# Kernel tuning notes

Measured on AMD Instinct MI355X. Metric: run time of the kernel, lower is better.

The kernel has to match this reference:

```python
import jax, jax.numpy as jnp
import numpy as np
import math

B, L, D = 2, 2048, 768
H, DK = 8, 64
DV = D // H  # 96
N_POS = 32
DFF = 2 * D
EPS = 1e-5


def setup_inputs() -> dict:
    key = jax.random.key(0)
    ks = jax.random.split(key, 12)
    s = 0.02
    return {
        "x": jax.random.normal(ks[0], (B, L, D), jnp.float32),
        "norm1_w": jnp.ones((D,), jnp.float32),
        "norm2_w": jnp.ones((D,), jnp.float32),
        "wq": jax.random.normal(ks[1], (D, H * DK), jnp.float32) * s,
        "wk": jax.random.normal(ks[2], (D, H * DK), jnp.float32) * s,
        "wv": jax.random.normal(ks[3], (D, H * DV), jnp.float32) * s,
        "wo": jax.random.normal(ks[4], (H * DV, D), jnp.float32) * s,
        "bo": jnp.zeros((D,), jnp.float32),
        "u_param": jax.random.normal(ks[5], (H, DK), jnp.float32) * s,
        "v_param": jax.random.normal(ks[6], (H, DK), jnp.float32) * s,
        "w_pos": jax.random.normal(ks[7], (H, DK, N_POS), jnp.float32) * s,
        "w1": jax.random.normal(ks[8], (D, DFF), jnp.float32) * s,
        "b1": jnp.zeros((DFF,), jnp.float32),
        "w2": jax.random.normal(ks[9], (DFF, D), jnp.float32) * s,
        "b2": jnp.zeros((D,), jnp.float32),
    }


def _rel_basis(l: int, n: int) -> jnp.ndarray:
    # Enformer-style central-mask relative position basis: [l, l, n]
    pos = jnp.arange(l)
    distance = pos[None, :] - pos[:, None]  # [l, l]
    pow_rate = jnp.exp(jnp.log(jnp.float32((l + 1) / 2.0)) / (n // 2))
    center_widths = pow_rate ** jnp.arange(1, n // 2 + 1, dtype=jnp.float32)
    d = distance[:, :, None].astype(jnp.float32)
    unsigned = (jnp.abs(d) <= center_widths).astype(jnp.float32)
    signed = jnp.sign(d) * unsigned
    return jnp.concatenate([unsigned, signed], axis=-1)  # [l, l, n]


def _rmsnorm(x, w):
    norm = jnp.mean(x * x, axis=-1, keepdims=True)
    return x * jax.lax.rsqrt(norm + EPS) * w


def reference(x, norm1_w, norm2_w, wq, wk, wv, wo, bo,
              u_param, v_param, w_pos, w1, b1, w2, b2):
    b, l, _ = x.shape
    skip = x
    h1 = _rmsnorm(x, norm1_w)

    q = (h1 @ wq).reshape(b, l, H, DK)
    k = (h1 @ wk).reshape(b, l, H, DK)
    v = (h1 @ wv).reshape(b, l, H, DV)

    basis = _rel_basis(l, N_POS)  # [l, l, n]
    scale = 1.0 / math.sqrt(DK)

    # qr_term: contract q with w_pos first, then with basis (avoids [h,l,l,d] r)
    qw = jnp.einsum('bihd,hdn->bihn', q, w_pos)          # [b,l,h,n]
    qr = jnp.einsum('bihn,ijn->bhij', qw, basis)          # [b,h,l,l]
    uk = jnp.einsum('hd,bjhd->bhj', u_param, k)[:, :, None, :]  # [b,h,1,l]
    vw = jnp.einsum('hd,hdn->hn', v_param, w_pos)         # [h,n]
    vr = jnp.einsum('hn,ijn->hij', vw, basis)[None]       # [1,h,l,l]

    bias = (qr + uk + vr) * scale
    scores = jnp.einsum('bihd,bjhd->bhij', q, k) * scale + bias
    attn = jax.nn.softmax(scores, axis=-1)
    out = jnp.einsum('bhij,bjhd->bihd', attn, v)          # [b,l,h,dv]

    out = out.reshape(b, l, H * DV) @ wo + bo
    x = out + skip

    skip = x
    h2 = _rmsnorm(x, norm2_w)
    h2 = jax.nn.gelu(h2 @ w1 + b1, approximate=False) @ w2 + b2
    return h2 + skip
```

## Files before the change

kernel.cpp:

```cpp
#include <hip/hip_runtime.h>

#define B_ 2
#define L_ 2048
#define D_ 768
#define H_ 8
#define DK_ 64
#define DV_ 96
#define NPOS_ 32

typedef __attribute__((ext_vector_type(8))) __bf16 bf16x8;
typedef __attribute__((ext_vector_type(4))) __bf16 bf16x4;
typedef __attribute__((ext_vector_type(4))) float f32x4;

static __device__ __forceinline__ float bs2f(short s) {
    return (float)__builtin_bit_cast(__bf16, s);
}
static __device__ __forceinline__ short f2bs(float f) {
    return __builtin_bit_cast(short, (__bf16)f);
}

typedef __attribute__((address_space(1))) void gas_void;
typedef __attribute__((address_space(3))) void las_void;
static __device__ __forceinline__ void gload16(const short* g, char* l) {
    __builtin_amdgcn_global_load_lds((const gas_void*)g, (las_void*)l, 16, 0, 0);
}

__global__ __launch_bounds__(256) void prep_kernel(
    const float* __restrict__ wq, const float* __restrict__ wk,
    const float* __restrict__ wv, const float* __restrict__ wo,
    const float* __restrict__ w1, const float* __restrict__ w2,
    const float* __restrict__ vparam, const float* __restrict__ uparam,
    const float* __restrict__ wpos,
    short* __restrict__ wqkvT, short* __restrict__ woT,
    short* __restrict__ w1T, short* __restrict__ w2T,
    unsigned char* __restrict__ sidx, float* __restrict__ VU, float* __restrict__ VS,
    const float* __restrict__ x, const float* __restrict__ n1w, short* __restrict__ h1)
{
    __shared__ short T[64][66];
    __shared__ float vw[H_ * NPOS_];
    __shared__ float uw[H_ * NPOS_];
    __shared__ float red[4];
    int blk = blockIdx.x, tid = threadIdx.x;
    if (blk < 1056) {
        const float* W; short* Wt; int K, N, bx, by;
        if (blk < 96)       { W = wq; Wt = wqkvT;              K = 768;  N = 512;  int b = blk;       bx = b % 8;  by = b / 8; }
        else if (blk < 192) { W = wk; Wt = wqkvT + 512 * 768;  K = 768;  N = 512;  int b = blk - 96;  bx = b % 8;  by = b / 8; }
        else if (blk < 336) { W = wv; Wt = wqkvT + 1024 * 768; K = 768;  N = 768;  int b = blk - 192; bx = b % 12; by = b / 12; }
        else if (blk < 480) { W = wo; Wt = woT;                K = 768;  N = 768;  int b = blk - 336; bx = b % 12; by = b / 12; }
        else if (blk < 768) { W = w1; Wt = w1T;                K = 768;  N = 1536; int b = blk - 480; bx = b % 24; by = b / 24; }
        else                { W = w2; Wt = w2T;                K = 1536; N = 768;  int b = blk - 768; bx = b % 12; by = b / 12; }
        int n0 = bx << 6, k0 = by << 6;
        for (int idx = tid; idx < 4096; idx += 256) {
            int r = idx >> 6, c = idx & 63;
            T[c][r] = f2bs(W[(size_t)(k0 + r) * N + n0 + c]);
        }
        __syncthreads();
        for (int idx = tid; idx < 4096; idx += 256) {
            int r = idx >> 6, c = idx & 63;
            Wt[(size_t)(n0 + r) * K + k0 + c] = T[r][c];
        }
    } else if (blk == 1056) {
        float pr = expf(logf((L_ + 1) / 2.0f) / (NPOS_ / 2));
        if (tid < 16) vw[tid] = powf(pr, (float)(tid + 1));
        __syncthreads();
        for (int idx = tid; idx < 4095; idx += 256) {
            int d = idx - 2047;
            int ad = d < 0 ? -d : d;
            int c = 0;
#pragma unroll
            for (int m = 0; m < 16; ++m)
                if (vw[m] < (float)ad) c++;
            sidx[idx] = (unsigned char)(d > 0 ? c : (d < 0 ? 17 + c : 34));
        }
        __syncthreads();
        {
            int h = tid >> 5, n = tid & 31;
            float av = 0.f, au = 0.f;
            for (int d = 0; d < DK_; ++d) {
                float wp = wpos[(h * DK_ + d) * NPOS_ + n];
                av += vparam[h * DK_ + d] * wp;
                au += uparam[h * DK_ + d] * wp;
            }
            vw[tid] = av;
            uw[tid] = au;
        }
        __syncthreads();
        if (tid < H_ * 17) {
            int h = tid / 17, m = tid % 17;
            float su = 0.f, ss = 0.f;
            for (int t2 = m; t2 < 16; ++t2) {
                su += vw[h * NPOS_ + t2] - uw[h * NPOS_ + t2];
                ss += vw[h * NPOS_ + 16 + t2] - uw[h * NPOS_ + 16 + t2];
            }
            VU[h * 17 + m] = su * 0.125f;
            VS[h * 17 + m] = ss * 0.125f;
        }
    } else {
        int row = blk - 1057;
        const float* xr = x + (size_t)row * D_;
        float ss = 0.f;
        for (int c = tid; c < D_; c += 256) { float f = xr[c]; ss += f * f; }
        for (int msk = 1; msk < 64; msk <<= 1) ss += __shfl_xor(ss, msk);
        if ((tid & 63) == 0) red[tid >> 6] = ss;
        __syncthreads();
        float tot = red[0] + red[1] + red[2] + red[3];
        float sc = rsqrtf(tot * (1.f / D_) + 1e-5f);
        for (int c = tid; c < D_; c += 256)
            h1[(size_t)row * D_ + c] = f2bs(xr[c] * sc * n1w[c]);
    }
}

__global__ __launch_bounds__(256) void rmsnorm_kernel(
    const float* __restrict__ x, const float* __restrict__ wgt, short* __restrict__ out)
{
    int row = blockIdx.x, tid = threadIdx.x;
    __shared__ float red[4];
    const float* xr = x + (size_t)row * D_;
    float ss = 0.f;
    for (int c = tid; c < D_; c += 256) { float f = xr[c]; ss += f * f; }
    for (int msk = 1; msk < 64; msk <<= 1) ss += __shfl_xor(ss, msk);
    if ((tid & 63) == 0) red[tid >> 6] = ss;
    __syncthreads();
    float tot = red[0] + red[1] + red[2] + red[3];
    float sc = rsqrtf(tot * (1.f / D_) + 1e-5f);
    for (int c = tid; c < D_; c += 256)
        out[(size_t)row * D_ + c] = f2bs(xr[c] * sc * wgt[c]);
}

template<int BN>
__global__ __launch_bounds__(512, 4) void gemmx(
    const short* __restrict__ A, const short* __restrict__ Bt,
    const float* __restrict__ bias, const float* __restrict__ uadd,
    const float* __restrict__ resid, void* __restrict__ outp,
    int M, int N, int K, int act, int out_f32)
{
    constexpr int STRIDE = 16384 + BN * 128;
    __shared__ __align__(16) char ldsb[2 * STRIDE];
    int tid = threadIdx.x;
    int w = tid >> 6, lane = tid & 63, quad = lane >> 4, t = lane & 15;
    int wm = (w >> 1) << 5;
    int wn = (w & 1) * (BN / 2);
    int m0b = blockIdx.y << 7, n0b = blockIdx.x * BN;

    int srow = tid >> 3;
    int scol = ((tid & 7) ^ (srow & 7)) << 3;
    const short* aSrc0 = A + (size_t)(m0b + srow) * K + scol;
    const short* aSrc1 = A + (size_t)(m0b + 64 + srow) * K + scol;
    const short* bSrc0 = Bt + (size_t)(n0b + srow) * K + scol;
    const short* bSrc1 = Bt + (size_t)(n0b + 64 + srow) * K + scol;
    int wo1024 = w << 10;

    f32x4 acc[2][BN / 32] = {};

    gload16(aSrc0, ldsb + wo1024);
    gload16(aSrc1, ldsb + 8192 + wo1024);
    gload16(bSrc0, ldsb + 16384 + wo1024);
    if (BN == 128) gload16(bSrc1, ldsb + 16384 + 8192 + wo1024);

    int swz = (t & 7) << 4;
    int cur = 0;
    for (int kb = 0; kb < K; kb += 64) {
        __syncthreads();
        if (kb + 64 < K) {
            char* nb = ldsb + (cur ^ 1) * STRIDE;
            gload16(aSrc0 + kb + 64, nb + wo1024);
            gload16(aSrc1 + kb + 64, nb + 8192 + wo1024);
            gload16(bSrc0 + kb + 64, nb + 16384 + wo1024);
            if (BN == 128) gload16(bSrc1 + kb + 64, nb + 16384 + 8192 + wo1024);
        }
        char* Ab = ldsb + cur * STRIDE;
        char* Bb = Ab + 16384;
#pragma unroll
        for (int ks = 0; ks < 2; ++ks) {
            int cb = ((ks << 6) + (quad << 4)) ^ swz;
            bf16x8 af[2], bf[BN / 32];
#pragma unroll
            for (int ms = 0; ms < 2; ++ms)
                af[ms] = *(const bf16x8*)(Ab + (wm + ms * 16 + t) * 128 + cb);
#pragma unroll
            for (int ns = 0; ns < BN / 32; ++ns)
                bf[ns] = *(const bf16x8*)(Bb + (wn + ns * 16 + t) * 128 + cb);
#pragma unroll
            for (int ms = 0; ms < 2; ++ms)
#pragma unroll
                for (int ns = 0; ns < BN / 32; ++ns)
                    acc[ms][ns] = __builtin_amdgcn_mfma_f32_16x16x32_bf16(af[ms], bf[ns], acc[ms][ns], 0, 0, 0);
        }
        cur ^= 1;
    }
#pragma unroll
    for (int ms = 0; ms < 2; ++ms)
#pragma unroll
        for (int ns = 0; ns < BN / 32; ++ns)
#pragma unroll
            for (int r = 0; r < 4; ++r) {
                int row = m0b + wm + ms * 16 + (quad << 2) + r;
                int col = n0b + wn + ns * 16 + t;
                float v2 = acc[ms][ns][r];
                if (uadd && col < 512) v2 = 0.125f * (v2 + uadd[col]);
                if (bias) v2 += bias[col];
                if (act == 1) v2 = 0.5f * v2 * (1.f + erff(v2 * 0.70710678118654752f));
                if (resid) v2 += resid[(size_t)row * N + col];
                if (out_f32) ((float*)outp)[(size_t)row * N + col] = v2;
                else ((short*)outp)[(size_t)row * N + col] = f2bs(v2);
            }
}

__global__ __launch_bounds__(256) void qv_kernel(
    const short* __restrict__ qkv, const float* __restrict__ wpos,
    const float* __restrict__ VU, const float* __restrict__ VS,
    float* __restrict__ Tg, short* __restrict__ vT, short* __restrict__ kT)
{
    __shared__ __align__(16) char arena[69696];
    int blk = blockIdx.x, tid = threadIdx.x;
    if (blk < 512) {
        float* qw = (float*)arena;
        float* sU = (float*)(arena + 1024);
        float* sS = (float*)(arena + 1568);
        int h = tid >> 5, n = tid & 31;
        float wlr[64];
#pragma unroll
        for (int d = 0; d < DK_; ++d)
            wlr[d] = wpos[(h * DK_ + d) * NPOS_ + n];
        int r0 = blk << 3;
        for (int rr = 0; rr < 8; ++rr) {
            int row = r0 + rr;
            const short* base = qkv + (size_t)row * 1792 + h * DK_;
            float acc = 0.f;
#pragma unroll
            for (int c8 = 0; c8 < 8; ++c8) {
                bf16x8 q8 = *(const bf16x8*)(base + (c8 << 3));
#pragma unroll
                for (int e = 0; e < 8; ++e)
                    acc += (float)q8[e] * wlr[(c8 << 3) + e];
            }
            qw[tid] = acc;
            __syncthreads();
            if (tid < 136) {
                int hh = tid / 17, m = tid % 17;
                float su = 0.f, ss = 0.f;
                for (int t2 = m; t2 < 16; ++t2) { su += qw[hh * NPOS_ + t2]; ss += qw[hh * NPOS_ + 16 + t2]; }
                sU[tid] = su + VU[tid];
                sS[tid] = ss + VS[tid];
            }
            __syncthreads();
            if (tid < 280) {
                int h2 = tid / 35, s = tid % 35;
                int m = s < 17 ? s : (s < 34 ? s - 17 : 0);
                float su = sU[h2 * 17 + m], ss = sS[h2 * 17 + m];
                Tg[(size_t)row * 280 + tid] = s < 17 ? su + ss : (s < 34 ? su - ss : su);
            }
        }
    } else if (blk < 768) {
        short* T = (short*)arena;
        int vb = blk - 512;
        int bh = vb >> 4, b = bh >> 3, h = bh & 7;
        int j0 = (vb & 15) << 7;
#pragma unroll
        for (int it = 0; it < 6; ++it) {
            int idx = tid + (it << 8);
            int row = idx / 12, c8 = (idx % 12) << 3;
            *(bf16x8*)&T[row * 104 + c8] =
                *(const bf16x8*)&qkv[(size_t)(b * L_ + j0 + row) * 1792 + 1024 + h * DV_ + c8];
        }
        __syncthreads();
#pragma unroll
        for (int it = 0; it < 6; ++it) {
            int idx = tid + (it << 8);
            int sub = idx / 768;
            int rem = idx - sub * 768;
            int f = rem >> 6, l = rem & 63;
            int dv = f >> 1, ks = f & 1;
            int q = l >> 4, t = l & 15;
            bf16x8 o;
#pragma unroll
            for (int e = 0; e < 8; ++e) {
                int jl = ((e & 3) << 4) + (ks << 3) + (q << 1) + (e >> 2);
                o[e] = __builtin_bit_cast(__bf16, T[(sub * 64 + jl) * 104 + dv * 16 + t]);
            }
            int jt = ((vb & 15) << 1) + sub;
            *(bf16x8*)&vT[((((size_t)bh * 32 + jt) * 12 + f) * 64 + l) * 8] = o;
        }
    } else {
        short* T = (short*)arena;
        int vb = blk - 768;
        int bh = vb >> 4, b = bh >> 3, h = bh & 7;
        int c128 = vb & 15;
        int j0 = c128 << 7;
#pragma unroll
        for (int it = 0; it < 4; ++it) {
            int idx = tid + (it << 8);
            int row = idx >> 3, c8 = (idx & 7) << 3;
            *(bf16x8*)&T[row * 72 + c8] =
                *(const bf16x8*)&qkv[(size_t)(b * L_ + j0 + row) * 1792 + 512 + h * DK_ + c8];
        }
        __syncthreads();
#pragma unroll
        for (int it = 0; it < 4; ++it) {
            int idx = tid + (it << 8);
            int sub = idx >> 9;
            int rem = idx & 511;
            int f = rem >> 6, l = rem & 63;
            int q = l >> 4, tt = l & 15;
            bf16x8 o = *(bf16x8*)&T[(sub * 64 + (f >> 1) * 16 + tt) * 72 + ((f & 1) << 5) + (q << 3)];
            int jt = (c128 << 1) + sub;
            *(bf16x8*)&kT[((((size_t)bh * 32 + jt) * 8 + f) * 64 + l) * 8] = o;
        }
    }
}

__global__ __launch_bounds__(256, 3) void flash_kernel(
    const short* __restrict__ qkv, const short* __restrict__ kT,
    const short* __restrict__ vT, const float* __restrict__ Tg,
    const unsigned char* __restrict__ sidx_g, short* __restrict__ ao)
{
    __shared__ __align__(16) char arena[27136];
    int tid = threadIdx.x;
    int w = tid >> 6, lane = tid & 63, quad = lane >> 4, t = lane & 15;
    short* Pla = (short*)(arena + w * 4608);
    short* Plb = (short*)(arena + w * 4608 + 2304);
    float* Tt = (float*)(arena + 18432);
    unsigned char* sidxl = (unsigned char*)(arena + 23040);

    int id = blockIdx.x;
    int bh8 = id & 7, rest = id >> 3;
    int x = rest & 63, hi = rest >> 6;
    int bh = bh8 + (hi << 3);
    int b = bh >> 3, h = bh & 7;
    int i0 = x << 5;

    for (int idx = tid; idx < 32 * 35; idx += 256) {
        int il = idx / 35, s = idx - il * 35;
        Tt[il * 36 + s] = Tg[(size_t)(b * L_ + i0 + il) * 280 + h * 35 + s];
    }
    for (int idx = tid; idx < 4095; idx += 256) sidxl[idx] = sidx_g[idx];
    __syncthreads();

    const short* qa = qkv + (size_t)(b * L_ + i0 + t) * 1792 + h * DK_;
    const short* qb = qkv + (size_t)(b * L_ + i0 + 16 + t) * 1792 + h * DK_;
    bf16x8 qf0a = *(const bf16x8*)(qa + (quad << 3));
    bf16x8 qf1a = *(const bf16x8*)(qa + 32 + (quad << 3));
    bf16x8 qf0b = *(const bf16x8*)(qb + (quad << 3));
    bf16x8 qf1b = *(const bf16x8*)(qb + 32 + (quad << 3));

    f32x4 Oa[6] = {}, Ob[6] = {};
    float lsa[4] = {0.f, 0.f, 0.f, 0.f};
    float lsb[4] = {0.f, 0.f, 0.f, 0.f};
    const short* kfb = kT + (size_t)bh * 32 * 8 * 512 + lane * 8;
    const short* vfb = vT + (size_t)bh * 32 * 12 * 512 + lane * 8;

    for (int tix = 0; tix < 8; ++tix) {
        int jt = (tix << 2) + w;
        int j0 = jt << 6;
        bf16x8 kf[8];
#pragma unroll
        for (int f = 0; f < 8; ++f)
            kf[f] = *(const bf16x8*)(kfb + ((size_t)jt * 8 + f) * 512);

        float bA[16];
#pragma unroll
        for (int r = 0; r < 4; ++r) {
            int il = (quad << 2) + r;
            int i = i0 + il;
            const float* Trow = &Tt[il * 36];
#pragma unroll
            for (int ct = 0; ct < 4; ++ct)
                bA[r * 4 + ct] = Trow[sidxl[j0 + ct * 16 + t - i + 2047]];
        }
        __builtin_amdgcn_sched_barrier(0);

        f32x4 S[4];
        __builtin_amdgcn_s_setprio(1);
#pragma unroll
        for (int ct = 0; ct < 4; ++ct) {
            f32x4 z = {};
            z = __builtin_amdgcn_mfma_f32_16x16x32_bf16(qf0a, kf[ct * 2], z, 0, 0, 0);
            S[ct] = __builtin_amdgcn_mfma_f32_16x16x32_bf16(qf1a, kf[ct * 2 + 1], z, 0, 0, 0);
        }
        __builtin_amdgcn_s_setprio(0);
#pragma unroll
        for (int r = 0; r < 4; ++r) {
            int il = (quad << 2) + r;
            bf16x4 pv;
#pragma unroll
            for (int ct = 0; ct < 4; ++ct) {
                float p = __expf(S[ct][r] + bA[r * 4 + ct]);
                __bf16 pb = (__bf16)p;
                pv[ct] = pb;
                lsa[r] += (float)pb;
            }
            *(bf16x4*)&Pla[il * 72 + t * 4] = pv;
        }
        float bB[16];
#pragma unroll
        for (int r = 0; r < 4; ++r) {
            int il = (quad << 2) + r;
            int i = i0 + 16 + il;
            const float* Trow = &Tt[(16 + il) * 36];
#pragma unroll
            for (int ct = 0; ct < 4; ++ct)
                bB[r * 4 + ct] = Trow[sidxl[j0 + ct * 16 + t - i + 2047]];
        }
        __builtin_amdgcn_s_setprio(1);
#pragma unroll
        for (int ct = 0; ct < 4; ++ct) {
            f32x4 z = {};
            z = __builtin_amdgcn_mfma_f32_16x16x32_bf16(qf0b, kf[ct * 2], z, 0, 0, 0);
            S[ct] = __builtin_amdgcn_mfma_f32_16x16x32_bf16(qf1b, kf[ct * 2 + 1], z, 0, 0, 0);
        }
        __builtin_amdgcn_s_setprio(0);

        bf16x8 vf[12];
#pragma unroll
        for (int f = 0; f < 12; ++f)
            vf[f] = *(const bf16x8*)(vfb + ((size_t)jt * 12 + f) * 512);
        __builtin_amdgcn_sched_barrier(0);
#pragma unroll
        for (int r = 0; r < 4; ++r) {
            int il = (quad << 2) + r;
            bf16x4 pv;
#pragma unroll
            for (int ct = 0; ct < 4; ++ct) {
                float p = __expf(S[ct][r] + bB[r * 4 + ct]);
                __bf16 pb = (__bf16)p;
                pv[ct] = pb;
                lsb[r] += (float)pb;
            }
            *(bf16x4*)&Plb[il * 72 + t * 4] = pv;
        }
        __builtin_amdgcn_s_setprio(1);
#pragma unroll
        for (int ks = 0; ks < 2; ++ks) {
            bf16x8 paa = *(bf16x8*)&Pla[t * 72 + (ks << 5) + (quad << 3)];
            bf16x8 pab = *(bf16x8*)&Plb[t * 72 + (ks << 5) + (quad << 3)];
#pragma unroll
            for (int dv = 0; dv < 6; ++dv) {
                Oa[dv] = __builtin_amdgcn_mfma_f32_16x16x32_bf16(paa, vf[dv * 2 + ks], Oa[dv], 0, 0, 0);
                Ob[dv] = __builtin_amdgcn_mfma_f32_16x16x32_bf16(pab, vf[dv * 2 + ks], Ob[dv], 0, 0, 0);
            }
        }
        __builtin_amdgcn_s_setprio(0);
    }

    float* F = (float*)arena;
#pragma unroll
    for (int g = 0; g < 2; ++g) {
        f32x4* O = g ? Ob : Oa;
        float* ls = g ? lsb : lsa;
        __syncthreads();
        if (w >= 2) {
            int col = ((w - 2) << 6) + lane;
#pragma unroll
            for (int dv = 0; dv < 6; ++dv)
#pragma unroll
                for (int r = 0; r < 4; ++r)
                    F[((dv << 2) + r) * 128 + col] = O[dv][r];
#pragma unroll
            for (int r = 0; r < 4; ++r) F[(24 + r) * 128 + col] = ls[r];
        }
        __syncthreads();
        if (w < 2) {
            int col = (w << 6) + lane;
#pragma unroll
            for (int dv = 0; dv < 6; ++dv)
#pragma unroll
                for (int r = 0; r < 4; ++r)
                    O[dv][r] += F[((dv << 2) + r) * 128 + col];
#pragma unroll
            for (int r = 0; r < 4; ++r) ls[r] += F[(24 + r) * 128 + col];
        }
        __syncthreads();
        if (w == 1) {
            int col = 64 + lane;
#pragma unroll
            for (int dv = 0; dv < 6; ++dv)
#pragma unroll
                for (int r = 0; r < 4; ++r)
                    F[((dv << 2) + r) * 128 + col] = O[dv][r];
#pragma unroll
            for (int r = 0; r < 4; ++r) F[(24 + r) * 128 + col] = ls[r];
        }
        __syncthreads();
        if (w == 0) {
            int col = 64 + lane;
#pragma unroll
            for (int r = 0; r < 4; ++r) {
                float lr = ls[r] + F[(24 + r) * 128 + col];
                lr += __shfl_xor(lr, 1);
                lr += __shfl_xor(lr, 2);
                lr += __shfl_xor(lr, 4);
                lr += __shfl_xor(lr, 8);
                float inv = 1.f / lr;
                int i = i0 + (g << 4) + (quad << 2) + r;
                size_t base = (size_t)(b * L_ + i) * D_ + h * DV_;
#pragma unroll
                for (int dv = 0; dv < 6; ++dv)
                    ao[base + dv * 16 + t] = f2bs((O[dv][r] + F[((dv << 2) + r) * 128 + col]) * inv);
            }
        }
    }
}

extern "C" void kernel_launch(void* const* d_in, const int* in_sizes, int n_in,
                              void* d_out, int out_size, void* d_ws, size_t ws_size,
                              hipStream_t stream)
{
    const float* x    = (const float*)d_in[0];
    const float* n1w  = (const float*)d_in[1];
    const float* n2w  = (const float*)d_in[2];
    const float* wq   = (const float*)d_in[3];
    const float* wk   = (const float*)d_in[4];
    const float* wv   = (const float*)d_in[5];
    const float* wo   = (const float*)d_in[6];
    const float* bo   = (const float*)d_in[7];
    const float* up   = (const float*)d_in[8];
    const float* vp   = (const float*)d_in[9];
    const float* wpos = (const float*)d_in[10];
    const float* w1   = (const float*)d_in[11];
    const float* b1   = (const float*)d_in[12];
    const float* w2   = (const float*)d_in[13];
    const float* b2   = (const float*)d_in[14];

    char* ws = (char*)d_ws;
    short* h1   = (short*)(ws + 0);
    short* qkv  = (short*)(ws + 6291456);
    float* Tg   = (float*)(ws + 20971520);
    float* VUg  = (float*)(ws + 25559040);
    float* VSg  = (float*)(ws + 25560064);
    unsigned char* sidx = (unsigned char*)(ws + 25561088);
    short* ao   = (short*)(ws + 25569280);
    float* x2   = (float*)(ws + 31860736);
    short* vT   = (short*)(ws + 31860736);
    short* kT   = (short*)(ws + 38152192);
    short* wqkvT= (short*)(ws + 44443648);
    short* woT  = (short*)(ws + 47196160);
    short* w1T  = (short*)(ws + 48375808);
    short* w2T  = (short*)(ws + 50735104);
    short* f1   = (short*)(ws + 0);
    short* h2n  = (short*)(ws + 14680064);

    prep_kernel<<<5153, 256, 0, stream>>>(wq, wk, wv, wo, w1, w2, vp, up, wpos,
                                          wqkvT, woT, w1T, w2T, sidx, VUg, VSg,
                                          x, n1w, h1);
    gemmx<128><<<dim3(14, 32), 512, 0, stream>>>(h1, wqkvT, nullptr, up, nullptr, qkv, 4096, 1792, 768, 0, 0);
    qv_kernel<<<1024, 256, 0, stream>>>(qkv, wpos, VUg, VSg, Tg, vT, kT);
    flash_kernel<<<dim3(1024), 256, 0, stream>>>(qkv, kT, vT, Tg, sidx, ao);
    gemmx<64><<<dim3(12, 32), 512, 0, stream>>>(ao, woT, bo, nullptr, x, x2, 4096, 768, 768, 0, 1);
    rmsnorm_kernel<<<4096, 256, 0, stream>>>(x2, n2w, h2n);
    gemmx<128><<<dim3(12, 32), 512, 0, stream>>>(h2n, w1T, b1, nullptr, nullptr, f1, 4096, 1536, 768, 1, 0);
    gemmx<64><<<dim3(12, 32), 512, 0, stream>>>(f1, w2T, b2, nullptr, x2, d_out, 4096, 768, 1536, 0, 1);
}
```

Baseline: 262.2 us.

## Triple-buffer GEMM K-loop with 32-wide tiles and explicit vmcnt waits

Result: slower. 277.1 us (+5.7%).

```diff
diff --git a/kernel.cpp b/kernel.cpp
--- a/kernel.cpp
+++ b/kernel.cpp
@@ -134,59 +134,65 @@
     const float* __restrict__ resid, void* __restrict__ outp,
     int M, int N, int K, int act, int out_f32)
 {
-    constexpr int STRIDE = 16384 + BN * 128;
-    __shared__ __align__(16) char ldsb[2 * STRIDE];
+    constexpr int BUF = 8192 + BN * 64;
+    __shared__ __align__(16) char ldsb[3 * BUF];
     int tid = threadIdx.x;
     int w = tid >> 6, lane = tid & 63, quad = lane >> 4, t = lane & 15;
     int wm = (w >> 1) << 5;
     int wn = (w & 1) * (BN / 2);
     int m0b = blockIdx.y << 7, n0b = blockIdx.x * BN;
 
-    int srow = tid >> 3;
-    int scol = ((tid & 7) ^ (srow & 7)) << 3;
-    const short* aSrc0 = A + (size_t)(m0b + srow) * K + scol;
-    const short* aSrc1 = A + (size_t)(m0b + 64 + srow) * K + scol;
-    const short* bSrc0 = Bt + (size_t)(n0b + srow) * K + scol;
-    const short* bSrc1 = Bt + (size_t)(n0b + 64 + srow) * K + scol;
-    int wo1024 = w << 10;
+    int srowA = tid >> 2;
+    int scA = ((tid & 3) ^ ((srowA >> 1) & 3)) << 3;
+    const short* aSrc = A + (size_t)(m0b + srowA) * K + scA;
+    int bw = (BN == 128) ? w : (w & 3);
+    int pt = (bw << 6) + lane;
+    int srowB = pt >> 2;
+    int scB = ((pt & 3) ^ ((srowB >> 1) & 3)) << 3;
+    const short* bSrc = Bt + (size_t)(n0b + srowB) * K + scB;
+    int aOff = w << 10;
+    int bOff = 8192 + (bw << 10);
 
     f32x4 acc[2][BN / 32] = {};
-
-    gload16(aSrc0, ldsb + wo1024);
-    gload16(aSrc1, ldsb + 8192 + wo1024);
-    gload16(bSrc0, ldsb + 16384 + wo1024);
-    if (BN == 128) gload16(bSrc1, ldsb + 16384 + 8192 + wo1024);
-
-    int swz = (t & 7) << 4;
-    int cur = 0;
-    for (int kb = 0; kb < K; kb += 64) {
-        __syncthreads();
-        if (kb + 64 < K) {
-            char* nb = ldsb + (cur ^ 1) * STRIDE;
-            gload16(aSrc0 + kb + 64, nb + wo1024);
-            gload16(aSrc1 + kb + 64, nb + 8192 + wo1024);
-            gload16(bSrc0 + kb + 64, nb + 16384 + wo1024);
-            if (BN == 128) gload16(bSrc1 + kb + 64, nb + 16384 + 8192 + wo1024);
-        }
-        char* Ab = ldsb + cur * STRIDE;
-        char* Bb = Ab + 16384;
-#pragma unroll
-        for (int ks = 0; ks < 2; ++ks) {
-            int cb = ((ks << 6) + (quad << 4)) ^ swz;
-            bf16x8 af[2], bf[BN / 32];
-#pragma unroll
-            for (int ms = 0; ms < 2; ++ms)
-                af[ms] = *(const bf16x8*)(Ab + (wm + ms * 16 + t) * 128 + cb);
+    int nIter = K >> 5;
+
+    gload16(aSrc, ldsb + aOff);
+    gload16(bSrc, ldsb + bOff);
+    gload16(aSrc + 32, ldsb + BUF + aOff);
+    gload16(bSrc + 32, ldsb + BUF + bOff);
+
+    char* p0 = ldsb;
+    char* p1 = ldsb + BUF;
+    char* p2 = ldsb + 2 * BUF;
+    for (int it = 0; it < nIter; ++it) {
+        if (it + 1 < nIter) {
+            asm volatile("s_waitcnt vmcnt(2)" ::: "memory");
+        } else {
+            asm volatile("s_waitcnt vmcnt(0)" ::: "memory");
+        }
+        __builtin_amdgcn_s_barrier();
+        int kn = (it + 2) << 5;
+        if (kn < K) {
+            gload16(aSrc + kn, p2 + aOff);
+            gload16(bSrc + kn, p2 + bOff);
+        }
+        bf16x8 af[2], bf[BN / 32];
+#pragma unroll
+        for (int ms = 0; ms < 2; ++ms) {
+            int R = wm + ms * 16 + t;
+            af[ms] = *(const bf16x8*)(p0 + R * 64 + (((quad ^ (R >> 1)) & 3) << 4));
+        }
+#pragma unroll
+        for (int ns = 0; ns < BN / 32; ++ns) {
+            int R = wn + ns * 16 + t;
+            bf[ns] = *(const bf16x8*)(p0 + 8192 + R * 64 + (((quad ^ (R >> 1)) & 3) << 4));
+        }
+#pragma unroll
+        for (int ms = 0; ms < 2; ++ms)
 #pragma unroll
             for (int ns = 0; ns < BN / 32; ++ns)
-                bf[ns] = *(const bf16x8*)(Bb + (wn + ns * 16 + t) * 128 + cb);
-#pragma unroll
-            for (int ms = 0; ms < 2; ++ms)
-#pragma unroll
-                for (int ns = 0; ns < BN / 32; ++ns)
-                    acc[ms][ns] = __builtin_amdgcn_mfma_f32_16x16x32_bf16(af[ms], bf[ns], acc[ms][ns], 0, 0, 0);
-        }
-        cur ^= 1;
+                acc[ms][ns] = __builtin_amdgcn_mfma_f32_16x16x32_bf16(af[ms], bf[ns], acc[ms][ns], 0, 0, 0);
+        char* tmp = p0; p0 = p1; p1 = p2; p2 = tmp;
     }
 #pragma unroll
     for (int ms = 0; ms < 2; ++ms)
```
